# Kernel tuning notes

Measured on AMD Instinct MI355X. Metric: run time of the kernel, lower is better.

## Reference

```python
import jax, jax.numpy as jnp
import numpy as np

# Multi-scale schedule for (T,H,W)=(1,16,16) from get_latent2scale_schedule
SCHEDULE = [(1, 1, 1), (1, 2, 2), (1, 3, 3), (1, 4, 4), (1, 5, 5),
            (1, 6, 6), (1, 8, 8), (1, 10, 10), (1, 13, 13), (1, 16, 16)]

N_EMBED = 196560  # Leech lattice kissing number
EMBED_DIM = 24


def _resize(x, thw):
    # x: [B, D, T, H, W] -> [B, D, t, h, w] (trilinear/bilinear interpolation)
    b, d = x.shape[:2]
    return jax.image.resize(x, (b, d) + tuple(thw), method='bilinear')


def _quantize(r, codebook):
    """SphericalVectorQuantizer with predefined (pre-normalized) codebook.
    r: [B, D, t, h, w].  d = -z @ codebook^T; argmin(d) == argmax(sim)."""
    b, d = r.shape[0], r.shape[1]
    spatial = r.shape[2:]
    zf = jnp.moveaxis(r, 1, -1).reshape(-1, d)            # [N, D] tokens
    sim = zf @ codebook.T                                  # [N, K] cosine similarity
    idx = jnp.argmax(jax.lax.stop_gradient(sim), axis=1)   # argmin of -sim
    zq = codebook[idx]                                     # gather [N, D]
    zq = zq / jnp.linalg.norm(zq, axis=-1, keepdims=True)  # F.normalize (no-op if unit)
    zq = zf + jax.lax.stop_gradient(zq - zf)               # straight-through estimator
    zq = jnp.moveaxis(zq.reshape((b,) + spatial + (d,)), -1, 1)
    return zq, idx


def setup_inputs() -> dict:
    key = jax.random.key(0)
    k1, k2 = jax.random.split(key)
    z = jax.random.normal(k1, (2, 24, 1, 16, 16), jnp.float32)
    cb = jax.random.normal(k2, (N_EMBED, EMBED_DIM), jnp.float32)
    cb = cb / jnp.linalg.norm(cb, axis=-1, keepdims=True)  # normalized Leech codebook
    return {"z": z, "codebook": cb}


def reference(z, codebook):
    # Multi-scale residual quantization (Algorithm 1, RQ-style):
    # downsample residual -> spherical VQ (STE) -> upsample -> accumulate/subtract.
    B, D, T, H, W = z.shape
    residual = z
    z_hat = jnp.zeros_like(z)
    all_idx = []
    for thw in SCHEDULE:
        r_down = _resize(residual, thw)
        zq, idx = _quantize(r_down, codebook)
        zq_up = _resize(zq, (T, H, W))
        z_hat = z_hat + zq_up
        residual = residual - jax.lax.stop_gradient(zq_up)  # residual detach (default)
        all_idx.append(idx)
    indices = jnp.concatenate(all_idx)  # [B * sum(t*h*w)] int codes
    return z_hat, indices
```

## Files before the change

### kernel.cpp

```cpp
#include <hip/hip_runtime.h>
#include <stdint.h>

#define KCB 196560
#define DIM 24
#define BB  2
#define ZEL 12288
#define NRB 384
#define RBS 512
#define NCTR 64
#define CSTR 64

typedef __attribute__((ext_vector_type(8)))  __bf16 bf16x8;
typedef __attribute__((ext_vector_type(16))) float  f32x16;

__device__ __forceinline__ unsigned long long pack_key(float sim, int idx) {
  unsigned u = __float_as_uint(sim);
  u = (u & 0x80000000u) ? ~u : (u | 0x80000000u);
  return ((unsigned long long)u << 32) | (unsigned)(~(unsigned)idx);
}

__device__ __forceinline__ void st_agent(float* p, float v) {
  __hip_atomic_store((unsigned*)p, __float_as_uint(v),
                     __ATOMIC_RELAXED, __HIP_MEMORY_SCOPE_AGENT);
}
__device__ __forceinline__ float ld_agent(const float* p) {
  return __uint_as_float(__hip_atomic_load((const unsigned*)p,
                         __ATOMIC_RELAXED, __HIP_MEMORY_SCOPE_AGENT));
}

__device__ __forceinline__ void bar_arrive(unsigned* ctr) {
  __syncthreads();
  if (threadIdx.x == 0)
    __hip_atomic_fetch_add(&ctr[(blockIdx.x & (NCTR - 1)) * CSTR], 1u,
                           __ATOMIC_RELAXED, __HIP_MEMORY_SCOPE_AGENT);
}
__device__ __forceinline__ void bar_wait(unsigned* ctr, unsigned NB) {
  if (threadIdx.x < 64) {
    while (true) {
      unsigned v = __hip_atomic_load(&ctr[threadIdx.x * CSTR],
                                     __ATOMIC_RELAXED, __HIP_MEMORY_SCOPE_AGENT);
      unsigned s = v;
#pragma unroll
      for (int d = 32; d; d >>= 1) s += __shfl_xor(s, d);
      if (s >= NB) break;
      __builtin_amdgcn_s_sleep(8);
    }
  }
  __syncthreads();
}

__global__ __launch_bounds__(256) void prep_kernel(const float* __restrict__ z,
    const float* __restrict__ cb, float* __restrict__ residual, float* __restrict__ out,
    float* __restrict__ rdown, ushort* __restrict__ th, ushort* __restrict__ tl,
    ushort* __restrict__ ch, ushort* __restrict__ cl, unsigned* __restrict__ ctr,
    int outTotal) {
  __shared__ float plane[256];
  int tid = threadIdx.x;
  int e = blockIdx.x * 256 + tid;
  if (e < outTotal) out[e] = 0.0f;
  for (int i = e; i < 20 * NCTR * CSTR; i += gridDim.x * 256) ctr[i] = 0u;
  if (e < KCB * 6) {
    int row = e / 6, q = e - row * 6;
    float4 v = *(const float4*)(cb + (size_t)row * 24 + q * 4);
    float xs[4] = {v.x, v.y, v.z, v.w};
    unsigned h[4], l[4];
#pragma unroll
    for (int k = 0; k < 4; ++k) {
      unsigned bits = __float_as_uint(xs[k]);
      h[k] = bits >> 16;
      float hif = __uint_as_float(bits & 0xffff0000u);
      l[k] = __float_as_uint(xs[k] - hif) >> 16;
    }
    *(uint2*)(ch + (size_t)row * 24 + q * 4) = make_uint2(h[0] | (h[1] << 16), h[2] | (h[3] << 16));
    *(uint2*)(cl + (size_t)row * 24 + q * 4) = make_uint2(l[0] | (l[1] << 16), l[2] | (l[3] << 16));
  }
  if (blockIdx.x < 48) {
    float v = z[e];
    residual[e] = v;
    plane[tid] = v;
    __syncthreads();
    if (tid == 0) {
      int t = 1;
      float inv_scale = 16.0f / (float)t;
      float ks = inv_scale;
      float sf_h = (0.0f + 0.5f) * inv_scale - 0.5f;
      float sf_w = (0.0f + 0.5f) * inv_scale - 0.5f;
      float wh[16], ww[16];
      float sh = 0.f, sw = 0.f;
#pragma unroll
      for (int i = 0; i < 16; ++i) {
        float vh = fmaxf(0.f, 1.f - fabsf(sf_h - (float)i) / ks);
        wh[i] = vh; sh += vh;
        float vw = fmaxf(0.f, 1.f - fabsf(sf_w - (float)i) / ks);
        ww[i] = vw; sw += vw;
      }
#pragma unroll
      for (int i = 0; i < 16; ++i) { wh[i] /= sh; ww[i] /= sw; }
      float acc = 0.f;
      for (int ih = 0; ih < 16; ++ih) {
        float ra = 0.f;
#pragma unroll
        for (int iw = 0; iw < 16; ++iw) ra = fmaf(ww[iw], plane[ih * 16 + iw], ra);
        acc = fmaf(wh[ih], ra, acc);
      }
      int b = blockIdx.x / DIM, d = blockIdx.x - (blockIdx.x / DIM) * DIM;
      int token = b;
      rdown[token * DIM + d] = acc;
      unsigned bits = __float_as_uint(acc);
      float hif = __uint_as_float(bits & 0xffff0000u);
      th[token * DIM + d] = (ushort)(bits >> 16);
      tl[token * DIM + d] = (ushort)(__float_as_uint(acc - hif) >> 16);
    }
  }
}

__device__ __forceinline__ void score_block(int rb, int tb, int T,
    const ushort* ch, const ushort* cl, const ushort* th, const ushort* tl,
    float* blockmax) {
  const int tid = threadIdx.x, lane = tid & 63, wv = tid >> 6;
  const int col = lane & 31, g = lane >> 5;
  const int tbase = tb * 128;
  const int ntt = min(4, (T - tbase + 31) >> 5);
  const uint4 z4 = make_uint4(0, 0, 0, 0);

  bf16x8 bh[4][2], bl[4][2];
#pragma unroll
  for (int tt = 0; tt < 4; ++tt) {
    int token = tbase + tt * 32 + col;
    bool tv = (tt < ntt) && (token < T);
    const ushort* tr = th + (size_t)token * 24;
    const ushort* sr = tl + (size_t)token * 24;
    uint4 h0 = tv ? *(const uint4*)(tr + g * 8) : z4;
    uint4 h1 = (tv && g == 0) ? *(const uint4*)(tr + 16) : z4;
    uint4 l0 = tv ? *(const uint4*)(sr + g * 8) : z4;
    uint4 l1 = (tv && g == 0) ? *(const uint4*)(sr + 16) : z4;
    bh[tt][0] = __builtin_bit_cast(bf16x8, h0);
    bh[tt][1] = __builtin_bit_cast(bf16x8, h1);
    bl[tt][0] = __builtin_bit_cast(bf16x8, l0);
    bl[tt][1] = __builtin_bit_cast(bf16x8, l1);
  }

  const f32x16 fzero = {};
  float runmax[4] = {-3.402823466e38f, -3.402823466e38f, -3.402823466e38f, -3.402823466e38f};
  const int rbase = rb * RBS + wv * 128;

#pragma unroll
  for (int rt = 0; rt < 4; ++rt) {
    int tilebase = rbase + rt * 32;
    if (tilebase >= KCB) continue;
    int row = tilebase + col;
    bool rv = row < KCB;
    const ushort* cr = ch + (size_t)row * 24;
    const ushort* dr = cl + (size_t)row * 24;
    uint4 a0 = rv ? *(const uint4*)(cr + g * 8) : z4;
    uint4 a1 = (rv && g == 0) ? *(const uint4*)(cr + 16) : z4;
    uint4 c0 = rv ? *(const uint4*)(dr + g * 8) : z4;
    uint4 c1 = (rv && g == 0) ? *(const uint4*)(dr + 16) : z4;
    bf16x8 ah0 = __builtin_bit_cast(bf16x8, a0);
    bf16x8 ah1 = __builtin_bit_cast(bf16x8, a1);
    bf16x8 al0 = __builtin_bit_cast(bf16x8, c0);
    bf16x8 al1 = __builtin_bit_cast(bf16x8, c1);
    int limit = KCB - tilebase;
    bool full = limit >= 32;
#pragma unroll
    for (int tt = 0; tt < 4; ++tt) {
      if (tt >= ntt) continue;
      f32x16 acc = __builtin_amdgcn_mfma_f32_32x32x16_bf16(ah0, bh[tt][0], fzero, 0, 0, 0);
      acc = __builtin_amdgcn_mfma_f32_32x32x16_bf16(ah1, bh[tt][1], acc, 0, 0, 0);
      acc = __builtin_amdgcn_mfma_f32_32x32x16_bf16(al0, bh[tt][0], acc, 0, 0, 0);
      acc = __builtin_amdgcn_mfma_f32_32x32x16_bf16(al1, bh[tt][1], acc, 0, 0, 0);
      acc = __builtin_amdgcn_mfma_f32_32x32x16_bf16(ah0, bl[tt][0], acc, 0, 0, 0);
      acc = __builtin_amdgcn_mfma_f32_32x32x16_bf16(ah1, bl[tt][1], acc, 0, 0, 0);
      float m;
      if (full) {
        float m01 = fmaxf(acc[0], acc[1]),  m23 = fmaxf(acc[2], acc[3]);
        float m45 = fmaxf(acc[4], acc[5]),  m67 = fmaxf(acc[6], acc[7]);
        float m89 = fmaxf(acc[8], acc[9]),  mab = fmaxf(acc[10], acc[11]);
        float mcd = fmaxf(acc[12], acc[13]), mef = fmaxf(acc[14], acc[15]);
        m = fmaxf(fmaxf(fmaxf(m01, m23), fmaxf(m45, m67)),
                  fmaxf(fmaxf(m89, mab), fmaxf(mcd, mef)));
      } else {
        m = -3.402823466e38f;
#pragma unroll
        for (int r = 0; r < 16; ++r) {
          int rowid = (r & 3) + 8 * (r >> 2) + 4 * g;
          if (rowid < limit) m = fmaxf(m, acc[r]);
        }
      }
      runmax[tt] = fmaxf(runmax[tt], m);
    }
  }

  __shared__ float lmax[4][4][32];
#pragma unroll
  for (int tt = 0; tt < 4; ++tt) {
    float v = fmaxf(runmax[tt], __shfl_xor(runmax[tt], 32));
    if (lane < 32) lmax[wv][tt][col] = v;
  }
  __syncthreads();
  if (tid < 128) {
    int tt = tid >> 5, c = tid & 31;
    if (tt < ntt) {
      float m = fmaxf(fmaxf(lmax[0][tt][c], lmax[1][tt][c]),
                      fmaxf(lmax[2][tt][c], lmax[3][tt][c]));
      int token = tbase + tt * 32 + c;
      if (token < T) st_agent(&blockmax[token * NRB + rb], m);
    }
  }
}

__device__ __forceinline__ void finalize_token(int tok, const float* __restrict__ cb,
    const float* rdown, const float* __restrict__ blockmax, float* __restrict__ zq_ws,
    float* __restrict__ out, int idxBase) {
  int lane = threadIdx.x & 63;
  float x = (lane < DIM) ? rdown[tok * DIM + lane] : 0.f;
  float av[DIM];
#pragma unroll
  for (int k = 0; k < DIM; ++k)
    av[k] = __uint_as_float(__builtin_amdgcn_readlane(__float_as_uint(x), k));
  float ss = 0.f;
#pragma unroll
  for (int k = 0; k < DIM; ++k) ss = fmaf(av[k], av[k], ss);
  float eps = 1e-3f * sqrtf(ss) + 1e-30f;

  const float* bmrow = blockmax + (size_t)tok * NRB;
  float bv[6];
#pragma unroll
  for (int i = 0; i < 6; ++i) bv[i] = ld_agent(&bmrow[lane + 64 * i]);
  float M = fmaxf(fmaxf(fmaxf(bv[0], bv[1]), fmaxf(bv[2], bv[3])), fmaxf(bv[4], bv[5]));
#pragma unroll
  for (int d = 32; d; d >>= 1) M = fmaxf(M, __shfl_xor(M, d));
  float thr = M - eps;

  unsigned long long bk = 0ull;
#pragma unroll
  for (int i = 0; i < 6; ++i) {
    unsigned long long mask = __ballot(bv[i] >= thr);
    while (mask) {
      int l = __ffsll((unsigned long long)mask) - 1;
      mask &= mask - 1;
      int rowb = (l + 64 * i) * RBS;
      for (int r8 = 0; r8 < 8; ++r8) {
        int row = rowb + r8 * 64 + lane;
        if (row < KCB) {
          const float* cv = cb + (size_t)row * DIM;
          float acc = 0.f;
#pragma unroll
          for (int k = 0; k < DIM; ++k) acc = fmaf(av[k], cv[k], acc);
          unsigned long long key = pack_key(acc, row);
          if (key > bk) bk = key;
        }
      }
    }
  }
#pragma unroll
  for (int d = 32; d; d >>= 1) {
    unsigned long long o = __shfl_xor(bk, d);
    if (o > bk) bk = o;
  }
  int idx = (int)(~(unsigned)bk);
  const float* cv = cb + (long long)idx * DIM;
  float xv = (lane < DIM) ? cv[lane] : 0.f;
  float v[DIM];
#pragma unroll
  for (int k = 0; k < DIM; ++k)
    v[k] = __uint_as_float(__builtin_amdgcn_readlane(__float_as_uint(xv), k));
  float s2 = 0.f;
#pragma unroll
  for (int k = 0; k < DIM; ++k) s2 = fmaf(v[k], v[k], s2);
  float nrm = sqrtf(s2);
  if (lane < DIM) st_agent(&zq_ws[tok * DIM + lane], xv / nrm);
  if (lane == 0) out[idxBase + tok] = (float)idx;
}

template<int TSZ, int TN>
__device__ __forceinline__ void update_plane(const float* __restrict__ zq_ws,
    float* residual, float* __restrict__ out, float* rdown, ushort* th, ushort* tl) {
  constexpr int N = TSZ * TSZ;
  int tid = threadIdx.x;
  int p = blockIdx.x;
  int b = p / DIM, d = p - b * DIM;
  __shared__ float ldsZ[256];
  __shared__ float plane[256];
  for (int sp = tid; sp < N; sp += 256) ldsZ[sp] = ld_agent(&zq_ws[(b * N + sp) * DIM + d]);
  __syncthreads();
  int e = p * 256 + tid;
  int w = e & 15, h = (e >> 4) & 15;
  float inv_scale = (float)TSZ / 16.0f;
  float sf_h = ((float)h + 0.5f) * inv_scale - 0.5f;
  float sf_w = ((float)w + 0.5f) * inv_scale - 0.5f;
  float wh[TSZ], ww[TSZ];
  float sh = 0.f, sw = 0.f;
#pragma unroll
  for (int j = 0; j < TSZ; ++j) {
    float vh = fmaxf(0.f, 1.f - fabsf(sf_h - (float)j));
    wh[j] = vh; sh += vh;
    float vw = fmaxf(0.f, 1.f - fabsf(sf_w - (float)j));
    ww[j] = vw; sw += vw;
  }
#pragma unroll
  for (int j = 0; j < TSZ; ++j) { wh[j] /= sh; ww[j] /= sw; }
  float acc = 0.f;
#pragma unroll
  for (int thh = 0; thh < TSZ; ++thh) {
    float ra = 0.f;
#pragma unroll
    for (int tw = 0; tw < TSZ; ++tw) ra = fmaf(ww[tw], ldsZ[thh * TSZ + tw], ra);
    acc = fmaf(wh[thh], ra, acc);
  }
  out[e] += acc;
  float rn = residual[e] - acc;
  residual[e] = rn;

  if constexpr (TN > 0) {
    plane[tid] = rn;
    __syncthreads();
    constexpr int n2 = TN * TN;
    for (int sp = tid; sp < n2; sp += 256) {
      int oh = sp / TN, ow = sp - oh * TN;
      float inv2 = 16.0f / (float)TN;
      float ks = inv2;
      float s_h = ((float)oh + 0.5f) * inv2 - 0.5f;
      float s_w = ((float)ow + 0.5f) * inv2 - 0.5f;
      float wh2[16], ww2[16];
      float sh2 = 0.f, sw2 = 0.f;
#pragma unroll
      for (int i = 0; i < 16; ++i) {
        float vh = fmaxf(0.f, 1.f - fabsf(s_h - (float)i) / ks);
        wh2[i] = vh; sh2 += vh;
        float vw = fmaxf(0.f, 1.f - fabsf(s_w - (float)i) / ks);
        ww2[i] = vw; sw2 += vw;
      }
#pragma unroll
      for (int i = 0; i < 16; ++i) { wh2[i] /= sh2; ww2[i] /= sw2; }
      float acc2 = 0.f;
      for (int ih = 0; ih < 16; ++ih) {
        float ra = 0.f;
#pragma unroll
        for (int iw = 0; iw < 16; ++iw) ra = fmaf(ww2[iw], plane[ih * 16 + iw], ra);
        acc2 = fmaf(wh2[ih], ra, acc2);
      }
      int token = b * n2 + sp;
      rdown[token * DIM + d] = acc2;
      unsigned bits = __float_as_uint(acc2);
      float hif = __uint_as_float(bits & 0xffff0000u);
      th[token * DIM + d] = (ushort)(bits >> 16);
      tl[token * DIM + d] = (ushort)(__float_as_uint(acc2 - hif) >> 16);
    }
  }
}

template<int TSZ, int TN>
__global__ __launch_bounds__(256) void step_kernel(
    const ushort* __restrict__ ch, const ushort* __restrict__ cl,
    ushort* th, ushort* tl,
    const float* __restrict__ cb, float* rdown,
    float* __restrict__ blockmax, float* __restrict__ zq_ws,
    float* residual, float* __restrict__ out,
    unsigned* __restrict__ ctrA, unsigned* __restrict__ ctrB, int idxBase) {
  constexpr int N = TSZ * TSZ;
  constexpr int T = BB * N;
  constexpr int NTB = (T + 127) / 128;
  constexpr unsigned NB_A = NRB * NTB;
  int tid = threadIdx.x;
  int wk = blockIdx.x;
  int rb = wk % NRB, tb = wk / NRB;

  score_block(rb, tb, T, ch, cl, th, tl, blockmax);
  bar_arrive(ctrA);
  if (blockIdx.x >= 48) return;

  bar_wait(ctrA, NB_A);
  {
    int wv = tid >> 6;
    for (int tok = blockIdx.x * 4 + wv; tok < T; tok += 192)
      finalize_token(tok, cb, rdown, blockmax, zq_ws, out, idxBase);
  }
  bar_arrive(ctrB);
  bar_wait(ctrB, 48u);

  update_plane<TSZ, TN>(zq_ws, residual, out, rdown, th, tl);
}

extern "C" void kernel_launch(void* const* d_in, const int* in_sizes, int n_in,
                              void* d_out, int out_size, void* d_ws, size_t ws_size,
                              hipStream_t stream) {
  const float* z  = (const float*)d_in[0];
  const float* cb = (const float*)d_in[1];
  float* out = (float*)d_out;
  float* residual = (float*)d_ws;
  float* rdown = residual + ZEL;
  float* blockmax = rdown + ZEL;
  unsigned long long* best =
      (unsigned long long*)(blockmax + 512 * NRB);
  ushort* th = (ushort*)(best + 512);
  ushort* tl = th + 512 * 24;
  ushort* ch = tl + 512 * 24;
  ushort* cl = ch + (size_t)KCB * 24;
  float* zq_ws = (float*)(cl + (size_t)KCB * 24);
  unsigned* ctr = (unsigned*)(zq_ws + 512 * 24);

  static const int TS[10] = {1, 2, 3, 4, 5, 6, 8, 10, 13, 16};

  prep_kernel<<<(KCB * 6 + 255) / 256, 256, 0, stream>>>(z, cb, residual, out, rdown,
                                                         th, tl, ch, cl, ctr, out_size);

  int prefix = 0;
  for (int s = 0; s < 10; ++s) {
    int t = TS[s], n = t * t, T = BB * n;
    int ntb = (T + 127) >> 7;
    int grid = NRB * ntb;
    int idxBase = ZEL + BB * prefix;
    unsigned* cA = ctr + (size_t)(2 * s + 0) * NCTR * CSTR;
    unsigned* cB = ctr + (size_t)(2 * s + 1) * NCTR * CSTR;
    switch (t) {
      case 1:  step_kernel<1,2><<<grid, 256, 0, stream>>>(ch, cl, th, tl, cb, rdown, blockmax, zq_ws, residual, out, cA, cB, idxBase); break;
      case 2:  step_kernel<2,3><<<grid, 256, 0, stream>>>(ch, cl, th, tl, cb, rdown, blockmax, zq_ws, residual, out, cA, cB, idxBase); break;
      case 3:  step_kernel<3,4><<<grid, 256, 0, stream>>>(ch, cl, th, tl, cb, rdown, blockmax, zq_ws, residual, out, cA, cB, idxBase); break;
      case 4:  step_kernel<4,5><<<grid, 256, 0, stream>>>(ch, cl, th, tl, cb, rdown, blockmax, zq_ws, residual, out, cA, cB, idxBase); break;
      case 5:  step_kernel<5,6><<<grid, 256, 0, stream>>>(ch, cl, th, tl, cb, rdown, blockmax, zq_ws, residual, out, cA, cB, idxBase); break;
      case 6:  step_kernel<6,8><<<grid, 256, 0, stream>>>(ch, cl, th, tl, cb, rdown, blockmax, zq_ws, residual, out, cA, cB, idxBase); break;
      case 8:  step_kernel<8,10><<<grid, 256, 0, stream>>>(ch, cl, th, tl, cb, rdown, blockmax, zq_ws, residual, out, cA, cB, idxBase); break;
      case 10: step_kernel<10,13><<<grid, 256, 0, stream>>>(ch, cl, th, tl, cb, rdown, blockmax, zq_ws, residual, out, cA, cB, idxBase); break;
      case 13: step_kernel<13,16><<<grid, 256, 0, stream>>>(ch, cl, th, tl, cb, rdown, blockmax, zq_ws, residual, out, cA, cB, idxBase); break;
      case 16: step_kernel<16,0><<<grid, 256, 0, stream>>>(ch, cl, th, tl, cb, rdown, blockmax, zq_ws, residual, out, cA, cB, idxBase); break;
    }
    prefix += n;
  }
}
```

Measured before the change: 365.3 us.

## Fuse all ten scale steps into one persistent kernel with grid barriers

Replaces the ten per-scale step kernel launches with a single persistent 768-block kernel that loops over scales and synchronises through global atomic barriers. Codebook row blocks are halved (256 rows per block, 768 blocks), and the bf16 hi/lo split of the tokens now happens per block in shared memory instead of being written to global memory. The aim is to remove launch overhead and launch gaps between scales. The cost is an extra grid-wide barrier per scale, the loss of compile-time scale templates in update_plane, and reliance on all 768 blocks being co-resident (launch_bounds 256,3).

```diff
diff --git a/kernel.cpp b/kernel.cpp
--- a/kernel.cpp
+++ b/kernel.cpp
@@ -5,13 +5,17 @@
 #define DIM 24
 #define BB  2
 #define ZEL 12288
-#define NRB 384
-#define RBS 512
+#define NRB 768
+#define RBS 256
+#define GRID 768
+#define NFIN 48
 #define NCTR 64
 #define CSTR 64
 
 typedef __attribute__((ext_vector_type(8)))  __bf16 bf16x8;
 typedef __attribute__((ext_vector_type(16))) float  f32x16;
+
+__device__ const int TS_d[10] = {1, 2, 3, 4, 5, 6, 8, 10, 13, 16};
 
 __device__ __forceinline__ unsigned long long pack_key(float sim, int idx) {
   unsigned u = __float_as_uint(sim);
@@ -51,14 +55,13 @@
 
 __global__ __launch_bounds__(256) void prep_kernel(const float* __restrict__ z,
     const float* __restrict__ cb, float* __restrict__ residual, float* __restrict__ out,
-    float* __restrict__ rdown, ushort* __restrict__ th, ushort* __restrict__ tl,
-    ushort* __restrict__ ch, ushort* __restrict__ cl, unsigned* __restrict__ ctr,
-    int outTotal) {
+    float* __restrict__ rdown, ushort* __restrict__ ch, ushort* __restrict__ cl,
+    unsigned* __restrict__ ctr, int outTotal) {
   __shared__ float plane[256];
   int tid = threadIdx.x;
   int e = blockIdx.x * 256 + tid;
   if (e < outTotal) out[e] = 0.0f;
-  for (int i = e; i < 20 * NCTR * CSTR; i += gridDim.x * 256) ctr[i] = 0u;
+  if (e < 32 * NCTR * CSTR) ctr[e] = 0u;
   if (e < KCB * 6) {
     int row = e / 6, q = e - row * 6;
     float4 v = *(const float4*)(cb + (size_t)row * 24 + q * 4);
@@ -104,36 +107,29 @@
         acc = fmaf(wh[ih], ra, acc);
       }
       int b = blockIdx.x / DIM, d = blockIdx.x - (blockIdx.x / DIM) * DIM;
-      int token = b;
-      rdown[token * DIM + d] = acc;
-      unsigned bits = __float_as_uint(acc);
-      float hif = __uint_as_float(bits & 0xffff0000u);
-      th[token * DIM + d] = (ushort)(bits >> 16);
-      tl[token * DIM + d] = (ushort)(__float_as_uint(acc - hif) >> 16);
-    }
-  }
-}
-
-__device__ __forceinline__ void score_block(int rb, int tb, int T,
-    const ushort* ch, const ushort* cl, const ushort* th, const ushort* tl,
-    float* blockmax) {
+      rdown[b * DIM + d] = acc;
+    }
+  }
+}
+
+__device__ __forceinline__ void score_tile(int rb, int tbase, int T,
+    const ushort* __restrict__ ch, const ushort* __restrict__ cl,
+    const ushort* tkh, const ushort* tkl, float (*lmax)[4][32], float* blockmax) {
   const int tid = threadIdx.x, lane = tid & 63, wv = tid >> 6;
   const int col = lane & 31, g = lane >> 5;
-  const int tbase = tb * 128;
-  const int ntt = min(4, (T - tbase + 31) >> 5);
+  const int nrem = T - tbase;
+  const int ntt = min(4, (nrem + 31) >> 5);
   const uint4 z4 = make_uint4(0, 0, 0, 0);
 
   bf16x8 bh[4][2], bl[4][2];
 #pragma unroll
   for (int tt = 0; tt < 4; ++tt) {
-    int token = tbase + tt * 32 + col;
-    bool tv = (tt < ntt) && (token < T);
-    const ushort* tr = th + (size_t)token * 24;
-    const ushort* sr = tl + (size_t)token * 24;
-    uint4 h0 = tv ? *(const uint4*)(tr + g * 8) : z4;
-    uint4 h1 = (tv && g == 0) ? *(const uint4*)(tr + 16) : z4;
-    uint4 l0 = tv ? *(const uint4*)(sr + g * 8) : z4;
-    uint4 l1 = (tv && g == 0) ? *(const uint4*)(sr + 16) : z4;
+    int lt = tt * 32 + col;
+    bool tv = (tt < ntt) && (lt < nrem);
+    uint4 h0 = tv ? *(const uint4*)(tkh + lt * 24 + g * 8) : z4;
+    uint4 h1 = (tv && g == 0) ? *(const uint4*)(tkh + lt * 24 + 16) : z4;
+    uint4 l0 = tv ? *(const uint4*)(tkl + lt * 24 + g * 8) : z4;
+    uint4 l1 = (tv && g == 0) ? *(const uint4*)(tkl + lt * 24 + 16) : z4;
     bh[tt][0] = __builtin_bit_cast(bf16x8, h0);
     bh[tt][1] = __builtin_bit_cast(bf16x8, h1);
     bl[tt][0] = __builtin_bit_cast(bf16x8, l0);
@@ -142,10 +138,10 @@
 
   const f32x16 fzero = {};
   float runmax[4] = {-3.402823466e38f, -3.402823466e38f, -3.402823466e38f, -3.402823466e38f};
-  const int rbase = rb * RBS + wv * 128;
-
-#pragma unroll
-  for (int rt = 0; rt < 4; ++rt) {
+  const int rbase = rb * RBS + wv * 64;
+
+#pragma unroll
+  for (int rt = 0; rt < 2; ++rt) {
     int tilebase = rbase + rt * 32;
     if (tilebase >= KCB) continue;
     int row = tilebase + col;
@@ -191,7 +187,6 @@
     }
   }
 
-  __shared__ float lmax[4][4][32];
 #pragma unroll
   for (int tt = 0; tt < 4; ++tt) {
     float v = fmaxf(runmax[tt], __shfl_xor(runmax[tt], 32));
@@ -213,7 +208,7 @@
     const float* rdown, const float* __restrict__ blockmax, float* __restrict__ zq_ws,
     float* __restrict__ out, int idxBase) {
   int lane = threadIdx.x & 63;
-  float x = (lane < DIM) ? rdown[tok * DIM + lane] : 0.f;
+  float x = (lane < DIM) ? ld_agent(&rdown[tok * DIM + lane]) : 0.f;
   float av[DIM];
 #pragma unroll
   for (int k = 0; k < DIM; ++k)
@@ -224,23 +219,25 @@
   float eps = 1e-3f * sqrtf(ss) + 1e-30f;
 
   const float* bmrow = blockmax + (size_t)tok * NRB;
-  float bv[6];
-#pragma unroll
-  for (int i = 0; i < 6; ++i) bv[i] = ld_agent(&bmrow[lane + 64 * i]);
-  float M = fmaxf(fmaxf(fmaxf(bv[0], bv[1]), fmaxf(bv[2], bv[3])), fmaxf(bv[4], bv[5]));
+  float bv[12];
+#pragma unroll
+  for (int i = 0; i < 12; ++i) bv[i] = ld_agent(&bmrow[lane + 64 * i]);
+  float M = bv[0];
+#pragma unroll
+  for (int i = 1; i < 12; ++i) M = fmaxf(M, bv[i]);
 #pragma unroll
   for (int d = 32; d; d >>= 1) M = fmaxf(M, __shfl_xor(M, d));
   float thr = M - eps;
 
   unsigned long long bk = 0ull;
 #pragma unroll
-  for (int i = 0; i < 6; ++i) {
+  for (int i = 0; i < 12; ++i) {
     unsigned long long mask = __ballot(bv[i] >= thr);
     while (mask) {
       int l = __ffsll((unsigned long long)mask) - 1;
       mask &= mask - 1;
       int rowb = (l + 64 * i) * RBS;
-      for (int r8 = 0; r8 < 8; ++r8) {
+      for (int r8 = 0; r8 < 4; ++r8) {
         int row = rowb + r8 * 64 + lane;
         if (row < KCB) {
           const float* cv = cb + (size_t)row * DIM;
@@ -273,113 +270,120 @@
   if (lane == 0) out[idxBase + tok] = (float)idx;
 }
 
-template<int TSZ, int TN>
-__device__ __forceinline__ void update_plane(const float* __restrict__ zq_ws,
-    float* residual, float* __restrict__ out, float* rdown, ushort* th, ushort* tl) {
-  constexpr int N = TSZ * TSZ;
+__device__ __forceinline__ void update_plane_rt(int tsz, int tnext,
+    const float* __restrict__ zq_ws, float* residual, float* __restrict__ out,
+    float* rdown, float* ldsZ, float* plane) {
+  int N = tsz * tsz;
   int tid = threadIdx.x;
   int p = blockIdx.x;
   int b = p / DIM, d = p - b * DIM;
-  __shared__ float ldsZ[256];
-  __shared__ float plane[256];
   for (int sp = tid; sp < N; sp += 256) ldsZ[sp] = ld_agent(&zq_ws[(b * N + sp) * DIM + d]);
   __syncthreads();
   int e = p * 256 + tid;
   int w = e & 15, h = (e >> 4) & 15;
-  float inv_scale = (float)TSZ / 16.0f;
+  float inv_scale = (float)tsz / 16.0f;
   float sf_h = ((float)h + 0.5f) * inv_scale - 0.5f;
   float sf_w = ((float)w + 0.5f) * inv_scale - 0.5f;
-  float wh[TSZ], ww[TSZ];
+  float wh[16], ww[16];
   float sh = 0.f, sw = 0.f;
-#pragma unroll
-  for (int j = 0; j < TSZ; ++j) {
+  for (int j = 0; j < tsz; ++j) {
     float vh = fmaxf(0.f, 1.f - fabsf(sf_h - (float)j));
     wh[j] = vh; sh += vh;
     float vw = fmaxf(0.f, 1.f - fabsf(sf_w - (float)j));
     ww[j] = vw; sw += vw;
   }
-#pragma unroll
-  for (int j = 0; j < TSZ; ++j) { wh[j] /= sh; ww[j] /= sw; }
+  for (int j = 0; j < tsz; ++j) { wh[j] /= sh; ww[j] /= sw; }
   float acc = 0.f;
-#pragma unroll
-  for (int thh = 0; thh < TSZ; ++thh) {
+  for (int thh = 0; thh < tsz; ++thh) {
     float ra = 0.f;
-#pragma unroll
-    for (int tw = 0; tw < TSZ; ++tw) ra = fmaf(ww[tw], ldsZ[thh * TSZ + tw], ra);
+    for (int tw = 0; tw < tsz; ++tw) ra = fmaf(ww[tw], ldsZ[thh * tsz + tw], ra);
     acc = fmaf(wh[thh], ra, acc);
   }
   out[e] += acc;
   float rn = residual[e] - acc;
   residual[e] = rn;
 
-  if constexpr (TN > 0) {
+  if (tnext > 0) {
     plane[tid] = rn;
     __syncthreads();
-    constexpr int n2 = TN * TN;
+    int n2 = tnext * tnext;
     for (int sp = tid; sp < n2; sp += 256) {
-      int oh = sp / TN, ow = sp - oh * TN;
-      float inv2 = 16.0f / (float)TN;
+      int oh = sp / tnext, ow = sp - oh * tnext;
+      float inv2 = 16.0f / (float)tnext;
       float ks = inv2;
       float s_h = ((float)oh + 0.5f) * inv2 - 0.5f;
       float s_w = ((float)ow + 0.5f) * inv2 - 0.5f;
       float wh2[16], ww2[16];
       float sh2 = 0.f, sw2 = 0.f;
-#pragma unroll
       for (int i = 0; i < 16; ++i) {
         float vh = fmaxf(0.f, 1.f - fabsf(s_h - (float)i) / ks);
         wh2[i] = vh; sh2 += vh;
         float vw = fmaxf(0.f, 1.f - fabsf(s_w - (float)i) / ks);
         ww2[i] = vw; sw2 += vw;
       }
-#pragma unroll
       for (int i = 0; i < 16; ++i) { wh2[i] /= sh2; ww2[i] /= sw2; }
       float acc2 = 0.f;
       for (int ih = 0; ih < 16; ++ih) {
         float ra = 0.f;
-#pragma unroll
         for (int iw = 0; iw < 16; ++iw) ra = fmaf(ww2[iw], plane[ih * 16 + iw], ra);
         acc2 = fmaf(wh2[ih], ra, acc2);
       }
-      int token = b * n2 + sp;
-      rdown[token * DIM + d] = acc2;
-      unsigned bits = __float_as_uint(acc2);
-      float hif = __uint_as_float(bits & 0xffff0000u);
-      th[token * DIM + d] = (ushort)(bits >> 16);
-      tl[token * DIM + d] = (ushort)(__float_as_uint(acc2 - hif) >> 16);
-    }
-  }
-}
-
-template<int TSZ, int TN>
-__global__ __launch_bounds__(256) void step_kernel(
+      st_agent(&rdown[(b * n2 + sp) * DIM + d], acc2);
+    }
+  }
+}
+
+__global__ __launch_bounds__(256, 3) void fused_kernel(
     const ushort* __restrict__ ch, const ushort* __restrict__ cl,
-    ushort* th, ushort* tl,
-    const float* __restrict__ cb, float* rdown,
-    float* __restrict__ blockmax, float* __restrict__ zq_ws,
-    float* residual, float* __restrict__ out,
-    unsigned* __restrict__ ctrA, unsigned* __restrict__ ctrB, int idxBase) {
-  constexpr int N = TSZ * TSZ;
-  constexpr int T = BB * N;
-  constexpr int NTB = (T + 127) / 128;
-  constexpr unsigned NB_A = NRB * NTB;
-  int tid = threadIdx.x;
-  int wk = blockIdx.x;
-  int rb = wk % NRB, tb = wk / NRB;
-
-  score_block(rb, tb, T, ch, cl, th, tl, blockmax);
-  bar_arrive(ctrA);
-  if (blockIdx.x >= 48) return;
-
-  bar_wait(ctrA, NB_A);
-  {
-    int wv = tid >> 6;
-    for (int tok = blockIdx.x * 4 + wv; tok < T; tok += 192)
-      finalize_token(tok, cb, rdown, blockmax, zq_ws, out, idxBase);
-  }
-  bar_arrive(ctrB);
-  bar_wait(ctrB, 48u);
-
-  update_plane<TSZ, TN>(zq_ws, residual, out, rdown, th, tl);
+    const float* __restrict__ cb,
+    float* rdown, float* blockmax, float* zq_ws,
+    float* residual, float* out, unsigned* ctr) {
+  __shared__ __align__(16) ushort tkh[128 * DIM];
+  __shared__ __align__(16) ushort tkl[128 * DIM];
+  __shared__ float lmax[4][4][32];
+  __shared__ float ldsZ[256];
+  __shared__ float plane[256];
+
+  const int tid = threadIdx.x;
+  const int bid = blockIdx.x;
+  int prefix = 0;
+  for (int s = 0; s < 10; ++s) {
+    const int t = TS_d[s];
+    const int n = t * t, T = BB * n;
+    const int ntb = (T + 127) >> 7;
+    unsigned* cA = ctr + (size_t)(3 * s + 0) * NCTR * CSTR;
+    unsigned* cB = ctr + (size_t)(3 * s + 1) * NCTR * CSTR;
+    unsigned* cC = ctr + (size_t)(3 * s + 2) * NCTR * CSTR;
+
+    for (int tb = 0; tb < ntb; ++tb) {
+      int tbase = tb * 128;
+      int ntok = min(128, T - tbase);
+      __syncthreads();
+      for (int i = tid; i < ntok * DIM; i += 256) {
+        float v = ld_agent(&rdown[tbase * DIM + i]);
+        unsigned bits = __float_as_uint(v);
+        tkh[i] = (ushort)(bits >> 16);
+        float hif = __uint_as_float(bits & 0xffff0000u);
+        tkl[i] = (ushort)(__float_as_uint(v - hif) >> 16);
+      }
+      __syncthreads();
+      score_tile(bid, tbase, T, ch, cl, tkh, tkl, lmax, blockmax);
+    }
+    bar_arrive(cA);
+
+    if (bid < NFIN) {
+      bar_wait(cA, GRID);
+      int wv = tid >> 6;
+      for (int tok = bid * 4 + wv; tok < T; tok += 4 * NFIN)
+        finalize_token(tok, cb, rdown, blockmax, zq_ws, out, ZEL + BB * prefix);
+      bar_arrive(cB);
+      bar_wait(cB, NFIN);
+      update_plane_rt(t, (s < 9) ? TS_d[s + 1] : 0, zq_ws, residual, out, rdown, ldsZ, plane);
+      bar_arrive(cC);
+    }
+    bar_wait(cC, NFIN);
+    prefix += n;
+  }
 }
 
 extern "C" void kernel_launch(void* const* d_in, const int* in_sizes, int n_in,
@@ -391,40 +395,13 @@
   float* residual = (float*)d_ws;
   float* rdown = residual + ZEL;
   float* blockmax = rdown + ZEL;
-  unsigned long long* best =
-      (unsigned long long*)(blockmax + 512 * NRB);
-  ushort* th = (ushort*)(best + 512);
-  ushort* tl = th + 512 * 24;
-  ushort* ch = tl + 512 * 24;
-  ushort* cl = ch + (size_t)KCB * 24;
-  float* zq_ws = (float*)(cl + (size_t)KCB * 24);
-  unsigned* ctr = (unsigned*)(zq_ws + 512 * 24);
-
-  static const int TS[10] = {1, 2, 3, 4, 5, 6, 8, 10, 13, 16};
+  float* zq_ws = blockmax + 512 * NRB;
+  unsigned* ctr = (unsigned*)(zq_ws + ZEL);
+  ushort* ch = (ushort*)(ctr + 32 * NCTR * CSTR);
+  ushort* cl = ch + (size_t)KCB * DIM;
 
   prep_kernel<<<(KCB * 6 + 255) / 256, 256, 0, stream>>>(z, cb, residual, out, rdown,
-                                                         th, tl, ch, cl, ctr, out_size);
-
-  int prefix = 0;
-  for (int s = 0; s < 10; ++s) {
-    int t = TS[s], n = t * t, T = BB * n;
-    int ntb = (T + 127) >> 7;
-    int grid = NRB * ntb;
-    int idxBase = ZEL + BB * prefix;
-    unsigned* cA = ctr + (size_t)(2 * s + 0) * NCTR * CSTR;
-    unsigned* cB = ctr + (size_t)(2 * s + 1) * NCTR * CSTR;
-    switch (t) {
-      case 1:  step_kernel<1,2><<<grid, 256, 0, stream>>>(ch, cl, th, tl, cb, rdown, blockmax, zq_ws, residual, out, cA, cB, idxBase); break;
-      case 2:  step_kernel<2,3><<<grid, 256, 0, stream>>>(ch, cl, th, tl, cb, rdown, blockmax, zq_ws, residual, out, cA, cB, idxBase); break;
-      case 3:  step_kernel<3,4><<<grid, 256, 0, stream>>>(ch, cl, th, tl, cb, rdown, blockmax, zq_ws, residual, out, cA, cB, idxBase); break;
-      case 4:  step_kernel<4,5><<<grid, 256, 0, stream>>>(ch, cl, th, tl, cb, rdown, blockmax, zq_ws, residual, out, cA, cB, idxBase); break;
-      case 5:  step_kernel<5,6><<<grid, 256, 0, stream>>>(ch, cl, th, tl, cb, rdown, blockmax, zq_ws, residual, out, cA, cB, idxBase); break;
-      case 6:  step_kernel<6,8><<<grid, 256, 0, stream>>>(ch, cl, th, tl, cb, rdown, blockmax, zq_ws, residual, out, cA, cB, idxBase); break;
-      case 8:  step_kernel<8,10><<<grid, 256, 0, stream>>>(ch, cl, th, tl, cb, rdown, blockmax, zq_ws, residual, out, cA, cB, idxBase); break;
-      case 10: step_kernel<10,13><<<grid, 256, 0, stream>>>(ch, cl, th, tl, cb, rdown, blockmax, zq_ws, residual, out, cA, cB, idxBase); break;
-      case 13: step_kernel<13,16><<<grid, 256, 0, stream>>>(ch, cl, th, tl, cb, rdown, blockmax, zq_ws, residual, out, cA, cB, idxBase); break;
-      case 16: step_kernel<16,0><<<grid, 256, 0, stream>>>(ch, cl, th, tl, cb, rdown, blockmax, zq_ws, residual, out, cA, cB, idxBase); break;
-    }
-    prefix += n;
-  }
-}
+                                                         ch, cl, ctr, out_size);
+  fused_kernel<<<GRID, 256, 0, stream>>>(ch, cl, cb, rdown, blockmax, zq_ws,
+                                         residual, out, ctr);
+}
```

After: 549.0 us. +50.3%, slower.
